# Optimization experiments

Measured on AMD Instinct MI355X. Metric: run time of the kernel, lower is better.

The kernel has to match this reference:

```python
import jax, jax.numpy as jnp
import numpy as np
from jax import lax

HUMAN_CONF = 0.7
IOU_TH = 0.5


def setup_inputs() -> dict:
    key = jax.random.key(0)
    k1, k2 = jax.random.split(key)
    B, Q, C = 16, 2048, 2
    return {
        "human_logits": jax.random.normal(k1, (B, Q, C), dtype=jnp.float32),
        "pred_boxes": jax.random.uniform(k2, (B, Q, 4), dtype=jnp.float32),  # cxcywh in [0,1]
        "img_h": 800,
        "img_w": 1333,
    }


def box_cxcywh_to_xyxy(b):
    cx, cy, w, h = b[..., 0], b[..., 1], b[..., 2], b[..., 3]
    return jnp.stack([cx - 0.5 * w, cy - 0.5 * h, cx + 0.5 * w, cy + 0.5 * h], axis=-1)


def pairwise_iou(b):
    # b: [Q,4] xyxy -> iou: [Q,Q]
    area = jnp.clip(b[:, 2] - b[:, 0], 0) * jnp.clip(b[:, 3] - b[:, 1], 0)
    lt = jnp.maximum(b[:, None, :2], b[None, :, :2])
    rb = jnp.minimum(b[:, None, 2:], b[None, :, 2:])
    wh = jnp.clip(rb - lt, 0)
    inter = wh[..., 0] * wh[..., 1]
    union = area[:, None] + area[None, :] - inter
    return inter / jnp.maximum(union, 1e-9)


def nms_keep(boxes, scores, valid, iou_th):
    # Greedy NMS on one image with fixed shapes; returns keep mask [Q].
    Q = scores.shape[0]
    order = jnp.argsort(jnp.where(valid, -scores, jnp.inf))  # valid boxes first, score desc
    b = boxes[order]
    v = valid[order]
    iou = pairwise_iou(b)                       # [Q,Q]
    idx = jnp.arange(Q)
    sup_mat = (iou > iou_th) & (idx[None, :] > idx[:, None])  # i suppresses later j

    def step(supp, i):
        keep_i = v[i] & jnp.logical_not(supp[i])
        supp = supp | (keep_i & sup_mat[i])
        return supp, keep_i

    _, keep_sorted = lax.scan(step, jnp.zeros(Q, bool), idx)
    return jnp.zeros(Q, bool).at[order].set(keep_sorted)


def reference(human_logits, pred_boxes, img_h, img_w):
    prob = jax.nn.softmax(human_logits, axis=-1)          # [B,Q,C]
    scores = prob.max(axis=-1)                            # [B,Q]
    labels = prob.argmax(axis=-1)                         # [B,Q]
    boxes = box_cxcywh_to_xyxy(pred_boxes)                # [B,Q,4]
    scale = jnp.array([img_w, img_h, img_w, img_h], dtype=boxes.dtype)
    boxes = boxes * scale
    valid = (labels == 0) & (scores >= HUMAN_CONF)
    keep = jax.vmap(lambda b, s, v: nms_keep(b, s, v, IOU_TH))(boxes, scores, valid)
    scores_out = jnp.where(keep, scores, 0.0)
    boxes_out = jnp.where(keep[..., None], boxes, 0.0).astype(jnp.int32)
    return scores_out, boxes_out, keep
```

## Files before the change

### kernel.cpp

```cpp
#include <hip/hip_runtime.h>
#include <math.h>


#define QN    2048
#define NS    1024
#define MATW  17408
#define MAGIC 0x5ca1ab1eu

#define REP32(X) X(0)X(1)X(2)X(3)X(4)X(5)X(6)X(7)X(8)X(9)X(10)X(11)X(12)X(13) \
                 X(14)X(15)X(16)X(17)X(18)X(19)X(20)X(21)X(22)X(23)X(24)X(25) \
                 X(26)X(27)X(28)X(29)X(30)X(31)

__device__ __forceinline__ int rb32(int wb) { return 64 * wb * (33 - wb); }

__device__ __forceinline__ unsigned long long shfl_xor_u64(unsigned long long x, int m) {
    int lo = __shfl_xor((int)(unsigned)(x & 0xffffffffull), m, 64);
    int hi = __shfl_xor((int)(unsigned)(x >> 32), m, 64);
    return ((unsigned long long)(unsigned)hi << 32) | (unsigned)lo;
}

__device__ __forceinline__ unsigned long long score_key(float2 l, int q, bool* valid_out) {
    float mx = fmaxf(l.x, l.y), mn = fminf(l.x, l.y);
    float e = expf(mn - mx);
    float score = 1.0f / (1.0f + e);
    bool valid = (l.x >= l.y) && (score >= 0.7f);
    *valid_out = valid;
    unsigned sbits = valid ? __float_as_uint(score) : 0u;
    return ((unsigned long long)(~sbits) << 32) | (unsigned)q;
}

__global__ __launch_bounds__(1024, 4) void kfused(
    const float* __restrict__ logits, const float* __restrict__ pboxes,
    const int* __restrict__ img_h_p, const int* __restrict__ img_w_p,
    unsigned* __restrict__ wflag, unsigned* __restrict__ wmat,
    float* __restrict__ out, int B)
{
    __shared__ __align__(16) char smem[41216];
    unsigned long long* skey = (unsigned long long*)smem;
    float* sx1 = (float*)(smem + 8192);
    float* sy1 = (float*)(smem + 12288);
    float* sx2 = (float*)(smem + 16384);
    float* sy2 = (float*)(smem + 20480);
    float* sar = (float*)(smem + 24576);
    unsigned short* sidxl = (unsigned short*)(smem + 28672);
    unsigned char* keepq = (unsigned char*)(smem + 30720);
    unsigned* skm = (unsigned*)(smem + 32768);
    int* sMp = (int*)(smem + 32896);
    unsigned long long* skeyB = (unsigned long long*)(smem + 33024);

    const int blk = blockIdx.x;
    const int b = blk % B, slice = blk / B;
    const int tid = threadIdx.x, lane = tid & 63, wave = tid >> 6;
    const float sw = (float)(*img_w_p), sh = (float)(*img_h_p);

    if (tid == 0) *sMp = 0;
    keepq[tid] = 0; keepq[tid + 1024] = 0;
    if (tid < 32) skm[tid] = 0;
    __syncthreads();

    const unsigned long long lmask_lt = (1ull << lane) - 1ull;
#pragma unroll
    for (int qq = 0; qq < 2; ++qq) {
        int q = tid + qq * 1024;
        float2 l = ((const float2*)logits)[b * QN + q];
        bool valid;
        unsigned long long key = score_key(l, q, &valid);
        unsigned long long mb = __ballot(valid);
        int base = 0;
        if (lane == 0 && mb) base = atomicAdd(sMp, __popcll(mb));
        base = __shfl(base, 0, 64);
        if (valid) {
            int slot = base + __popcll(mb & lmask_lt);
            if (slot < NS) skey[slot] = key;
        }
    }
    __syncthreads();
    const int M = *sMp;

    if (M <= NS) {
        unsigned long long v = (tid < M) ? skey[tid] : ~0ull;
        __syncthreads();
#pragma unroll
        for (int k = 2; k <= 64; k <<= 1) {
            bool dir = ((tid & k) == 0);
#pragma unroll
            for (int j = k >> 1; j > 0; j >>= 1) {
                unsigned long long o = shfl_xor_u64(v, j);
                bool takeMin = (dir == ((tid & j) == 0));
                v = ((v < o) == takeMin) ? v : o;
            }
        }
        int pp = 0;
        for (int k = 128; k <= NS; k <<= 1) {
            bool dir = ((tid & k) == 0);
            for (int j = k >> 1; j >= 64; j >>= 1) {
                unsigned long long* buf = pp ? skeyB : skey;
                pp ^= 1;
                buf[tid] = v;
                __syncthreads();
                unsigned long long o = buf[tid ^ j];
                bool takeMin = (dir == ((tid & j) == 0));
                v = ((v < o) == takeMin) ? v : o;
            }
#pragma unroll
            for (int j = 32; j > 0; j >>= 1) {
                unsigned long long o = shfl_xor_u64(v, j);
                bool takeMin = (dir == ((tid & j) == 0));
                v = ((v < o) == takeMin) ? v : o;
            }
        }
        int qi = (int)((unsigned)v & 0xffffu);
        sidxl[tid] = (unsigned short)qi;
        float x1 = 0.f, y1 = 0.f, x2 = 0.f, y2 = 0.f, ar = 0.f;
        if (tid < M) {
            float4 pb = ((const float4*)pboxes)[b * QN + qi];
            x1 = (pb.x - 0.5f * pb.z) * sw;
            y1 = (pb.y - 0.5f * pb.w) * sh;
            x2 = (pb.x + 0.5f * pb.z) * sw;
            y2 = (pb.y + 0.5f * pb.w) * sh;
            ar = fmaxf(x2 - x1, 0.f) * fmaxf(y2 - y1, 0.f);
        }
        sx1[tid] = x1; sy1[tid] = y1; sx2[tid] = x2; sy2[tid] = y2; sar[tid] = ar;
        __syncthreads();

        unsigned* mat = wmat + (long)b * MATW;
        const int NG = (M + 3) >> 2;
        const int W64 = (M + 63) >> 6;
        for (int gi = slice * 16 + wave; gi < NG; gi += 128) {
            const int g = gi << 2;
            const int nr = min(4, M - g);
            const int wb = g >> 6;
            const int rl = 32 - 2 * wb;
            float ax1[4], ay1[4], ax2[4], ay2[4], aar[4];
            int rbase[4];
#pragma unroll
            for (int r = 0; r < 4; ++r) {
                int i = g + min(r, nr - 1);
                ax1[r] = sx1[i]; ay1[r] = sy1[i];
                ax2[r] = sx2[i]; ay2[r] = sy2[i]; aar[r] = sar[i];
                rbase[r] = rb32(wb) + ((g + r) & 63) * rl;
            }
            for (int w = wb; w < W64; ++w) {
                int j = (w << 6) | lane;
                float bx1 = sx1[j], by1 = sy1[j], bx2 = sx2[j], by2 = sy2[j], bar = sar[j];
#pragma unroll
                for (int r = 0; r < 4; ++r) {
                    float ltx = fmaxf(ax1[r], bx1), lty = fmaxf(ay1[r], by1);
                    float rbx = fminf(ax2[r], bx2), rby = fminf(ay2[r], by2);
                    float wx = fmaxf(rbx - ltx, 0.f), wy = fmaxf(rby - lty, 0.f);
                    float inter = wx * wy;
                    float uni = aar[r] + bar - inter;
                    float iou = inter / fmaxf(uni, 1e-9f);
                    bool sup = (iou > 0.5f) && (j > g + r);
                    unsigned long long bal = __ballot(sup);
                    if (lane == 0 && r < nr)
                        *(unsigned long long*)(mat + rbase[r] + 2 * (w - wb)) = bal;
                }
            }
        }
        __syncthreads();
        if (tid == 0)
            __hip_atomic_store(&wflag[b * 8 + slice], MAGIC,
                               __ATOMIC_RELEASE, __HIP_MEMORY_SCOPE_AGENT);
        if (slice != 0) return;

        if (wave == 0) {
            const unsigned* fp = &wflag[b * 8 + (lane & 7)];
            for (;;) {
                unsigned f = (lane < 8)
                    ? __hip_atomic_load(fp, __ATOMIC_ACQUIRE, __HIP_MEMORY_SCOPE_AGENT)
                    : MAGIC;
                if (__all(f == MAGIC)) break;
                __builtin_amdgcn_s_sleep(2);
            }
            const unsigned* gm = wmat + (long)b * MATW;
            unsigned rem = 0;
            const int Ms = __builtin_amdgcn_readfirstlane(M);
            const int C = (Ms + 31) >> 5;
#define DECLV(t) unsigned rr##t = 0u, nn##t = 0u;
            REP32(DECLV)
#undef DECLV
            if (C > 0) {
                int Lc = min(tid, 31);
#define LD0(t) rr##t = gm[Lc + t * 32];
                REP32(LD0)
#undef LD0
            }
            for (int c = 0; c < C; ++c) {
                if (c + 1 < C) {
                    int cn = c + 1, wbn = cn >> 1, rln = 32 - 2 * wbn;
                    int Lcn = min(max(tid, 2 * wbn), 31);
                    int rb0n = rb32(wbn) + ((cn & 1) << 5) * rln + (Lcn - 2 * wbn);
#define LDN(t) nn##t = gm[rb0n + t * rln];
                    REP32(LDN)
#undef LDN
                }
                unsigned rw = (unsigned)__builtin_amdgcn_readlane((int)rem, c);
                unsigned keepmask = 0;
                int lim = min(32, Ms - (c << 5));
#define STEP(t) if (t < lim && !((rw >> t) & 1u)) {                         \
                    keepmask |= (1u << t);                                   \
                    rem |= rr##t;                                            \
                    rw |= (unsigned)__builtin_amdgcn_readlane((int)rr##t, c); }
                REP32(STEP)
#undef STEP
                if (tid == 0) skm[c] = keepmask;
                if (c + 1 < C) {
#define CPYV(t) rr##t = nn##t;
                    REP32(CPYV)
#undef CPYV
                }
            }
        }
        __syncthreads();
        for (int s = tid; s < M; s += 1024)
            if ((skm[s >> 5] >> (s & 31)) & 1u) keepq[sidxl[s]] = 1;
        __syncthreads();
    } else {
        if (slice != 0) return;
        unsigned long long* skeyF = (unsigned long long*)smem;
        unsigned char* ssupp = (unsigned char*)(smem + 16384);
        for (int q = tid; q < QN; q += 1024) {
            float2 l = ((const float2*)logits)[b * QN + q];
            bool valid;
            skeyF[q] = score_key(l, q, &valid);
        }
        __syncthreads();
        for (int k = 2; k <= QN; k <<= 1)
            for (int j = k >> 1; j > 0; j >>= 1) {
                int i = ((tid & ~(j - 1)) << 1) | (tid & (j - 1));
                int p = i | j;
                bool up = ((i & k) == 0);
                unsigned long long a = skeyF[i], c2 = skeyF[p];
                if ((a > c2) == up) { skeyF[i] = c2; skeyF[p] = a; }
                __syncthreads();
            }
        for (int s = tid; s < M; s += 1024) ssupp[s] = 0;
        __syncthreads();
        for (int i = 0; i < M; ++i) {
            __syncthreads();
            if (ssupp[i]) continue;
            int ia = (unsigned short)(unsigned)skeyF[i];
            float4 pa = ((const float4*)pboxes)[b * QN + ia];
            float ax1 = (pa.x - 0.5f * pa.z) * sw, ay1 = (pa.y - 0.5f * pa.w) * sh;
            float ax2 = (pa.x + 0.5f * pa.z) * sw, ay2 = (pa.y + 0.5f * pa.w) * sh;
            float areaA = fmaxf(ax2 - ax1, 0.f) * fmaxf(ay2 - ay1, 0.f);
            for (int jj = i + 1 + tid; jj < M; jj += 1024) {
                int jb = (unsigned short)(unsigned)skeyF[jj];
                float4 pq = ((const float4*)pboxes)[b * QN + jb];
                float bx1 = (pq.x - 0.5f * pq.z) * sw, by1 = (pq.y - 0.5f * pq.w) * sh;
                float bx2 = (pq.x + 0.5f * pq.z) * sw, by2 = (pq.y + 0.5f * pq.w) * sh;
                float ltx = fmaxf(ax1, bx1), lty = fmaxf(ay1, by1);
                float rbx = fminf(ax2, bx2), rby = fminf(ay2, by2);
                float wx = fmaxf(rbx - ltx, 0.f), wy = fmaxf(rby - lty, 0.f);
                float inter = wx * wy;
                float areaB = fmaxf(bx2 - bx1, 0.f) * fmaxf(by2 - by1, 0.f);
                float uni = areaA + areaB - inter;
                if (inter / fmaxf(uni, 1e-9f) > 0.5f) ssupp[jj] = 1;
            }
        }
        __syncthreads();
        for (int s = tid; s < M; s += 1024)
            if (!ssupp[s]) keepq[(unsigned short)(unsigned)skeyF[s]] = 1;
        __syncthreads();
    }

    const long BQ = (long)B * QN;
#pragma unroll
    for (int qq = 0; qq < 2; ++qq) {
        int q = tid + qq * 1024;
        int base = b * QN + q;
        float2 l = ((const float2*)logits)[base];
        float e = expf(fminf(l.x, l.y) - fmaxf(l.x, l.y));
        float score = 1.0f / (1.0f + e);
        float4 pb = ((const float4*)pboxes)[base];
        float x1 = (pb.x - 0.5f * pb.z) * sw, y1 = (pb.y - 0.5f * pb.w) * sh;
        float x2 = (pb.x + 0.5f * pb.z) * sw, y2 = (pb.y + 0.5f * pb.w) * sh;
        int kp = keepq[q];
        out[base] = kp ? score : 0.f;
        out[BQ * 5 + base] = kp ? 1.f : 0.f;
        float4 ob;
        ob.x = kp ? truncf(x1) : 0.f;
        ob.y = kp ? truncf(y1) : 0.f;
        ob.z = kp ? truncf(x2) : 0.f;
        ob.w = kp ? truncf(y2) : 0.f;
        ((float4*)(out + BQ))[base] = ob;
    }
}

extern "C" void kernel_launch(void* const* d_in, const int* in_sizes, int n_in,
                              void* d_out, int out_size, void* d_ws, size_t ws_size,
                              hipStream_t stream) {
    const float* logits = (const float*)d_in[0];
    const float* pboxes = (const float*)d_in[1];
    const int*   img_h  = (const int*)d_in[2];
    const int*   img_w  = (const int*)d_in[3];
    float* out = (float*)d_out;
    const int B = in_sizes[0] / (QN * 2);

    char* ws = (char*)d_ws;
    unsigned* wflag = (unsigned*)(ws + 0);
    unsigned* wmat  = (unsigned*)(ws + 1024);

    kfused<<<dim3(B * 8), dim3(1024), 0, stream>>>(logits, pboxes, img_h, img_w,
                                                   wflag, wmat, out, B);
}
```

Baseline: 103.1 us.

## Double NMS slices per image and use diagonal-word greedy scan

Launches 16 blocks per image instead of 8, so the IoU bitmask construction is spread over twice as many workgroups, and the flag wait polls 16 slice flags. The serial greedy scan also changes: instead of 32 predicated steps per chunk, it loads a per-lane diagonal mask word and iterates only over surviving candidates using ctz and readlane. The suppression rows are then merged using the final keep mask. This cuts serial latency in the single-wave scan, at the cost of more blocks spinning on flags and an extra load per chunk.

```diff
diff --git a/kernel.cpp b/kernel.cpp
--- a/kernel.cpp
+++ b/kernel.cpp
@@ -2,10 +2,11 @@
 #include <math.h>
 
 
-#define QN    2048
-#define NS    1024
-#define MATW  17408
-#define MAGIC 0x5ca1ab1eu
+#define QN     2048
+#define NS     1024
+#define NSLICE 16
+#define MATW   17408
+#define MAGIC  0x5ca1ab1eu
 
 #define REP32(X) X(0)X(1)X(2)X(3)X(4)X(5)X(6)X(7)X(8)X(9)X(10)X(11)X(12)X(13) \
                  X(14)X(15)X(16)X(17)X(18)X(19)X(20)X(21)X(22)X(23)X(24)X(25) \
@@ -126,7 +127,7 @@
         unsigned* mat = wmat + (long)b * MATW;
         const int NG = (M + 3) >> 2;
         const int W64 = (M + 63) >> 6;
-        for (int gi = slice * 16 + wave; gi < NG; gi += 128) {
+        for (int gi = slice * 16 + wave; gi < NG; gi += 256) {
             const int g = gi << 2;
             const int nr = min(4, M - g);
             const int wb = g >> 6;
@@ -160,14 +161,14 @@
         }
         __syncthreads();
         if (tid == 0)
-            __hip_atomic_store(&wflag[b * 8 + slice], MAGIC,
+            __hip_atomic_store(&wflag[b * NSLICE + slice], MAGIC,
                                __ATOMIC_RELEASE, __HIP_MEMORY_SCOPE_AGENT);
         if (slice != 0) return;
 
         if (wave == 0) {
-            const unsigned* fp = &wflag[b * 8 + (lane & 7)];
+            const unsigned* fp = &wflag[b * NSLICE + (lane & (NSLICE - 1))];
             for (;;) {
-                unsigned f = (lane < 8)
+                unsigned f = (lane < NSLICE)
                     ? __hip_atomic_load(fp, __ATOMIC_ACQUIRE, __HIP_MEMORY_SCOPE_AGENT)
                     : MAGIC;
                 if (__all(f == MAGIC)) break;
@@ -177,14 +178,16 @@
             unsigned rem = 0;
             const int Ms = __builtin_amdgcn_readfirstlane(M);
             const int C = (Ms + 31) >> 5;
+            const int lam = min(tid, 31);
+            unsigned diag = 0, diagN = 0;
 #define DECLV(t) unsigned rr##t = 0u, nn##t = 0u;
             REP32(DECLV)
 #undef DECLV
             if (C > 0) {
-                int Lc = min(tid, 31);
-#define LD0(t) rr##t = gm[Lc + t * 32];
+#define LD0(t) rr##t = gm[lam + t * 32];
                 REP32(LD0)
 #undef LD0
+                diag = gm[lam * 32];
             }
             for (int c = 0; c < C; ++c) {
                 if (c + 1 < C) {
@@ -194,21 +197,29 @@
 #define LDN(t) nn##t = gm[rb0n + t * rln];
                     REP32(LDN)
 #undef LDN
+                    diagN = gm[rb32(wbn) + (((cn & 1) << 5) + lam) * rln + (cn - 2 * wbn)];
                 }
                 unsigned rw = (unsigned)__builtin_amdgcn_readlane((int)rem, c);
+                int lim = min(32, Ms - (c << 5));
+                unsigned limmask = (lim >= 32) ? 0xFFFFFFFFu : ((1u << lim) - 1u);
+                unsigned avail = (~rw) & limmask;
                 unsigned keepmask = 0;
-                int lim = min(32, Ms - (c << 5));
-#define STEP(t) if (t < lim && !((rw >> t) & 1u)) {                         \
-                    keepmask |= (1u << t);                                   \
-                    rem |= rr##t;                                            \
-                    rw |= (unsigned)__builtin_amdgcn_readlane((int)rr##t, c); }
-                REP32(STEP)
-#undef STEP
+                while (avail) {
+                    int t = __builtin_ctz(avail);
+                    keepmask |= (1u << t);
+                    unsigned rword = (unsigned)__builtin_amdgcn_readlane((int)diag, t);
+                    avail &= ~(1u << t);
+                    avail &= ~rword;
+                }
+#define MRG(t) rem |= (0u - ((keepmask >> t) & 1u)) & rr##t;
+                REP32(MRG)
+#undef MRG
                 if (tid == 0) skm[c] = keepmask;
                 if (c + 1 < C) {
 #define CPYV(t) rr##t = nn##t;
                     REP32(CPYV)
 #undef CPYV
+                    diag = diagN;
                 }
             }
         }
@@ -302,6 +313,6 @@
     unsigned* wflag = (unsigned*)(ws + 0);
     unsigned* wmat  = (unsigned*)(ws + 1024);
 
-    kfused<<<dim3(B * 8), dim3(1024), 0, stream>>>(logits, pboxes, img_h, img_w,
-                                                   wflag, wmat, out, B);
+    kfused<<<dim3(B * NSLICE), dim3(1024), 0, stream>>>(logits, pboxes, img_h, img_w,
+                                                        wflag, wmat, out, B);
 }
```

Result: no change. 103.3 us (+0.2%).
